# Kernel tuning notes

Measured on AMD Instinct MI355X. Metric: run time of the kernel, lower is better.

Reference implementation:

```python
import jax, jax.numpy as jnp
import numpy as np

GAMMA = 12.0
EMB_INIT = 0.05


def setup_inputs() -> dict:
    key = jax.random.key(0)
    k1, k2, k3 = jax.random.split(key, 3)
    num_chunks, chunk_size, neg_sample_size, hidden_dim = 4, 512, 256, 512
    heads = jax.random.normal(k1, (num_chunks * chunk_size, hidden_dim), dtype=jnp.float32)
    relations = jax.random.normal(k2, (num_chunks * chunk_size, hidden_dim // 2), dtype=jnp.float32)
    tails = jax.random.normal(k3, (num_chunks * neg_sample_size, hidden_dim), dtype=jnp.float32)
    return {
        "heads": heads,
        "relations": relations,
        "tails": tails,
        "num_chunks": num_chunks,
        "chunk_size": chunk_size,
        "neg_sample_size": neg_sample_size,
    }


def reference(heads, relations, tails, num_chunks, chunk_size, neg_sample_size):
    # RotatE tail-negative scoring (create_neg with neg_head=False)
    hidden_dim = heads.shape[1]
    h = hidden_dim // 2
    re_head, im_head = heads[:, :h], heads[:, h:]
    # rotate head by relation phase
    phase_rel = relations / (EMB_INIT / np.pi)
    rel_real, rel_imag = jnp.cos(phase_rel), jnp.sin(phase_rel)
    real = re_head * rel_real - im_head * rel_imag  # [nc*cs, h]
    imag = re_head * rel_imag + im_head * rel_real
    # broadcast subtract against negative tails
    tmp_r = real.reshape(num_chunks, chunk_size, 1, h)
    tmp_i = imag.reshape(num_chunks, chunk_size, 1, h)
    tails4 = tails.reshape(num_chunks, 1, neg_sample_size, hidden_dim)
    t_r, t_i = tails4[..., :h], tails4[..., h:]
    dr = tmp_r - t_r  # [nc, cs, ns, h]
    di = tmp_i - t_i
    score = jnp.sqrt(dr * dr + di * di).sum(-1)  # [nc, cs, ns]
    return GAMMA - score
```

## Files before the change

kernel.cpp:

```cpp
#include <hip/hip_runtime.h>

#define NC 4
#define CS 512
#define NS 256
#define HD 512
#define H  256
#define GAMMA_F 12.0f
#define PHASE_SCALE 62.83185307179586477f

#define KT 16

__global__ __launch_bounds__(256, 2) void score_partial(
    const float* __restrict__ heads,
    const float* __restrict__ relations,
    const float* __restrict__ tails,
    float* __restrict__ part)
{
    __shared__ float2 sh[64][KT + 1];
    __shared__ float2 st[64][KT + 1];

    int bid = blockIdx.x;
    int c    = bid >> 7;
    int rem  = bid & 127;
    int ks   = rem >> 5;
    int rem2 = rem & 31;
    int hT   = rem2 >> 2;
    int tT   = rem2 & 3;

    int hBase = c * CS + hT * 64;
    int tBase = c * NS + tT * 64;
    int kSlice = ks * 64;

    int tid = threadIdx.x;
    int tx = tid & 15;
    int ty = tid >> 4;

    int srow = tid >> 2;
    int sk   = (tid & 3) * 4;

    float acc[4][4];
    #pragma unroll
    for (int m = 0; m < 4; ++m)
        #pragma unroll
        for (int n = 0; n < 4; ++n) acc[m][n] = 0.f;

    for (int r = 0; r < 64 / KT; ++r) {
        int kBase = kSlice + r * KT;

        const float* hp = heads + (size_t)(hBase + srow) * HD + kBase + sk;
        float4 hre = *reinterpret_cast<const float4*>(hp);
        float4 him = *reinterpret_cast<const float4*>(hp + H);
        float4 rel = *reinterpret_cast<const float4*>(
            relations + (size_t)(hBase + srow) * H + kBase + sk);
        const float* tp = tails + (size_t)(tBase + srow) * HD + kBase + sk;
        float4 tre = *reinterpret_cast<const float4*>(tp);
        float4 tim = *reinterpret_cast<const float4*>(tp + H);

        __syncthreads();

        {
            float s, cc;
            __sincosf(rel.x * PHASE_SCALE, &s, &cc);
            sh[srow][sk + 0] = make_float2(hre.x * cc - him.x * s,
                                           hre.x * s + him.x * cc);
            __sincosf(rel.y * PHASE_SCALE, &s, &cc);
            sh[srow][sk + 1] = make_float2(hre.y * cc - him.y * s,
                                           hre.y * s + him.y * cc);
            __sincosf(rel.z * PHASE_SCALE, &s, &cc);
            sh[srow][sk + 2] = make_float2(hre.z * cc - him.z * s,
                                           hre.z * s + him.z * cc);
            __sincosf(rel.w * PHASE_SCALE, &s, &cc);
            sh[srow][sk + 3] = make_float2(hre.w * cc - him.w * s,
                                           hre.w * s + him.w * cc);
        }
        st[srow][sk + 0] = make_float2(tre.x, tim.x);
        st[srow][sk + 1] = make_float2(tre.y, tim.y);
        st[srow][sk + 2] = make_float2(tre.z, tim.z);
        st[srow][sk + 3] = make_float2(tre.w, tim.w);

        __syncthreads();

        #pragma unroll
        for (int kk = 0; kk < KT; ++kk) {
            float2 hv[4], tv[4];
            hv[0] = sh[ty     ][kk];
            hv[1] = sh[ty + 16][kk];
            hv[2] = sh[ty + 32][kk];
            hv[3] = sh[ty + 48][kk];
            tv[0] = st[tx     ][kk];
            tv[1] = st[tx + 16][kk];
            tv[2] = st[tx + 32][kk];
            tv[3] = st[tx + 48][kk];
            #pragma unroll
            for (int m = 0; m < 4; ++m) {
                #pragma unroll
                for (int n = 0; n < 4; ++n) {
                    float dr = hv[m].x - tv[n].x;
                    float di = hv[m].y - tv[n].y;
                    acc[m][n] += __builtin_amdgcn_sqrtf(dr * dr + di * di);
                }
            }
        }
    }

    float* plane = part + (size_t)ks * (NC * CS * NS);
    size_t cbase = (size_t)c * CS * NS;
    #pragma unroll
    for (int m = 0; m < 4; ++m) {
        int i0 = hT * 64 + ty + 16 * m;
        #pragma unroll
        for (int n = 0; n < 4; ++n) {
            int j0 = tT * 64 + tx + 16 * n;
            plane[cbase + (size_t)i0 * NS + j0] = acc[m][n];
        }
    }
}

__global__ __launch_bounds__(256) void reduce_kernel(
    const float* __restrict__ part, float* __restrict__ out)
{
    const int PLANE = NC * CS * NS;
    int idx = (blockIdx.x * 256 + threadIdx.x) * 4;
    float4 p0 = *reinterpret_cast<const float4*>(part + idx);
    float4 p1 = *reinterpret_cast<const float4*>(part + PLANE + idx);
    float4 p2 = *reinterpret_cast<const float4*>(part + 2 * PLANE + idx);
    float4 p3 = *reinterpret_cast<const float4*>(part + 3 * PLANE + idx);
    float4 r;
    r.x = GAMMA_F - (p0.x + p1.x + p2.x + p3.x);
    r.y = GAMMA_F - (p0.y + p1.y + p2.y + p3.y);
    r.z = GAMMA_F - (p0.z + p1.z + p2.z + p3.z);
    r.w = GAMMA_F - (p0.w + p1.w + p2.w + p3.w);
    *reinterpret_cast<float4*>(out + idx) = r;
}

extern "C" void kernel_launch(void* const* d_in, const int* in_sizes, int n_in,
                              void* d_out, int out_size, void* d_ws, size_t ws_size,
                              hipStream_t stream) {
    (void)in_sizes; (void)n_in; (void)ws_size; (void)out_size;
    const float* heads = (const float*)d_in[0];
    const float* rels  = (const float*)d_in[1];
    const float* tails = (const float*)d_in[2];
    float* part = (float*)d_ws;

    score_partial<<<512, 256, 0, stream>>>(heads, rels, tails, part);
    reduce_kernel<<<512, 256, 0, stream>>>(part, (float*)d_out);
}
```

Baseline: 99.69 us.

## Drop split-K partial planes; use 32x32 tiles with full-K loop and prefetch

```diff
diff --git a/kernel.cpp b/kernel.cpp
--- a/kernel.cpp
+++ b/kernel.cpp
@@ -8,55 +8,48 @@
 #define GAMMA_F 12.0f
 #define PHASE_SCALE 62.83185307179586477f
 
-#define KT 16
+#define KT 32
+#define NR (H / KT)
 
-__global__ __launch_bounds__(256, 2) void score_partial(
+__global__ __launch_bounds__(256, 2) void rotate_score(
     const float* __restrict__ heads,
     const float* __restrict__ relations,
     const float* __restrict__ tails,
-    float* __restrict__ part)
+    float* __restrict__ out)
 {
-    __shared__ float2 sh[64][KT + 1];
-    __shared__ float2 st[64][KT + 1];
+    __shared__ float2 sh[32][KT + 1];
+    __shared__ float2 st[32][KT + 1];
 
-    int bid = blockIdx.x;
-    int c    = bid >> 7;
-    int rem  = bid & 127;
-    int ks   = rem >> 5;
-    int rem2 = rem & 31;
-    int hT   = rem2 >> 2;
-    int tT   = rem2 & 3;
+    const int bid = blockIdx.x;
+    const int c   = bid >> 7;
+    const int rem = bid & 127;
+    const int hT  = rem >> 3;
+    const int tT  = rem & 7;
 
-    int hBase = c * CS + hT * 64;
-    int tBase = c * NS + tT * 64;
-    int kSlice = ks * 64;
+    const int hBase = c * CS + hT * 32;
+    const int tBase = c * NS + tT * 32;
 
-    int tid = threadIdx.x;
-    int tx = tid & 15;
-    int ty = tid >> 4;
+    const int tid = threadIdx.x;
+    const int tx  = tid & 15;
+    const int ty  = tid >> 4;
 
-    int srow = tid >> 2;
-    int sk   = (tid & 3) * 4;
+    const int srow = tid >> 3;
+    const int sk   = (tid & 7) * 4;
 
-    float acc[4][4];
-    #pragma unroll
-    for (int m = 0; m < 4; ++m)
-        #pragma unroll
-        for (int n = 0; n < 4; ++n) acc[m][n] = 0.f;
+    const float* hp0 = heads     + (size_t)(hBase + srow) * HD + sk;
+    const float* rp0 = relations + (size_t)(hBase + srow) * H  + sk;
+    const float* tp0 = tails     + (size_t)(tBase + srow) * HD + sk;
 
-    for (int r = 0; r < 64 / KT; ++r) {
-        int kBase = kSlice + r * KT;
+    float4 hre = *reinterpret_cast<const float4*>(hp0);
+    float4 him = *reinterpret_cast<const float4*>(hp0 + H);
+    float4 rel = *reinterpret_cast<const float4*>(rp0);
+    float4 tre = *reinterpret_cast<const float4*>(tp0);
+    float4 tim = *reinterpret_cast<const float4*>(tp0 + H);
 
-        const float* hp = heads + (size_t)(hBase + srow) * HD + kBase + sk;
-        float4 hre = *reinterpret_cast<const float4*>(hp);
-        float4 him = *reinterpret_cast<const float4*>(hp + H);
-        float4 rel = *reinterpret_cast<const float4*>(
-            relations + (size_t)(hBase + srow) * H + kBase + sk);
-        const float* tp = tails + (size_t)(tBase + srow) * HD + kBase + sk;
-        float4 tre = *reinterpret_cast<const float4*>(tp);
-        float4 tim = *reinterpret_cast<const float4*>(tp + H);
+    float acc00 = 0.f, acc01 = 0.f, acc10 = 0.f, acc11 = 0.f;
 
-        __syncthreads();
+    for (int r = 0; r < NR; ++r) {
+        if (r) __syncthreads();
 
         {
             float s, cc;
@@ -80,68 +73,49 @@
 
         __syncthreads();
 
+        if (r + 1 < NR) {
+            const int kOff = (r + 1) * KT;
+            hre = *reinterpret_cast<const float4*>(hp0 + kOff);
+            him = *reinterpret_cast<const float4*>(hp0 + H + kOff);
+            rel = *reinterpret_cast<const float4*>(rp0 + kOff);
+            tre = *reinterpret_cast<const float4*>(tp0 + kOff);
+            tim = *reinterpret_cast<const float4*>(tp0 + H + kOff);
+        }
+
         #pragma unroll
         for (int kk = 0; kk < KT; ++kk) {
-            float2 hv[4], tv[4];
-            hv[0] = sh[ty     ][kk];
-            hv[1] = sh[ty + 16][kk];
-            hv[2] = sh[ty + 32][kk];
-            hv[3] = sh[ty + 48][kk];
-            tv[0] = st[tx     ][kk];
-            tv[1] = st[tx + 16][kk];
-            tv[2] = st[tx + 32][kk];
-            tv[3] = st[tx + 48][kk];
-            #pragma unroll
-            for (int m = 0; m < 4; ++m) {
-                #pragma unroll
-                for (int n = 0; n < 4; ++n) {
-                    float dr = hv[m].x - tv[n].x;
-                    float di = hv[m].y - tv[n].y;
-                    acc[m][n] += __builtin_amdgcn_sqrtf(dr * dr + di * di);
-                }
-            }
+            float2 h0 = sh[ty     ][kk];
+            float2 h1 = sh[ty + 16][kk];
+            float2 t0 = st[tx     ][kk];
+            float2 t1 = st[tx + 16][kk];
+            float dr, di;
+            dr = h0.x - t0.x; di = h0.y - t0.y;
+            acc00 += __builtin_amdgcn_sqrtf(fmaf(dr, dr, di * di));
+            dr = h0.x - t1.x; di = h0.y - t1.y;
+            acc01 += __builtin_amdgcn_sqrtf(fmaf(dr, dr, di * di));
+            dr = h1.x - t0.x; di = h1.y - t0.y;
+            acc10 += __builtin_amdgcn_sqrtf(fmaf(dr, dr, di * di));
+            dr = h1.x - t1.x; di = h1.y - t1.y;
+            acc11 += __builtin_amdgcn_sqrtf(fmaf(dr, dr, di * di));
         }
     }
 
-    float* plane = part + (size_t)ks * (NC * CS * NS);
-    size_t cbase = (size_t)c * CS * NS;
-    #pragma unroll
-    for (int m = 0; m < 4; ++m) {
-        int i0 = hT * 64 + ty + 16 * m;
-        #pragma unroll
-        for (int n = 0; n < 4; ++n) {
-            int j0 = tT * 64 + tx + 16 * n;
-            plane[cbase + (size_t)i0 * NS + j0] = acc[m][n];
-        }
-    }
-}
-
-__global__ __launch_bounds__(256) void reduce_kernel(
-    const float* __restrict__ part, float* __restrict__ out)
-{
-    const int PLANE = NC * CS * NS;
-    int idx = (blockIdx.x * 256 + threadIdx.x) * 4;
-    float4 p0 = *reinterpret_cast<const float4*>(part + idx);
-    float4 p1 = *reinterpret_cast<const float4*>(part + PLANE + idx);
-    float4 p2 = *reinterpret_cast<const float4*>(part + 2 * PLANE + idx);
-    float4 p3 = *reinterpret_cast<const float4*>(part + 3 * PLANE + idx);
-    float4 r;
-    r.x = GAMMA_F - (p0.x + p1.x + p2.x + p3.x);
-    r.y = GAMMA_F - (p0.y + p1.y + p2.y + p3.y);
-    r.z = GAMMA_F - (p0.z + p1.z + p2.z + p3.z);
-    r.w = GAMMA_F - (p0.w + p1.w + p2.w + p3.w);
-    *reinterpret_cast<float4*>(out + idx) = r;
+    const size_t cbase = (size_t)c * CS * NS;
+    const int i0 = hT * 32 + ty;
+    const int j0 = tT * 32 + tx;
+    out[cbase + (size_t)i0        * NS + j0     ] = GAMMA_F - acc00;
+    out[cbase + (size_t)i0        * NS + j0 + 16] = GAMMA_F - acc01;
+    out[cbase + (size_t)(i0 + 16) * NS + j0     ] = GAMMA_F - acc10;
+    out[cbase + (size_t)(i0 + 16) * NS + j0 + 16] = GAMMA_F - acc11;
 }
 
 extern "C" void kernel_launch(void* const* d_in, const int* in_sizes, int n_in,
                               void* d_out, int out_size, void* d_ws, size_t ws_size,
                               hipStream_t stream) {
-    (void)in_sizes; (void)n_in; (void)ws_size; (void)out_size;
+    (void)in_sizes; (void)n_in; (void)ws_size; (void)out_size; (void)d_ws;
     const float* heads = (const float*)d_in[0];
     const float* rels  = (const float*)d_in[1];
     const float* tails = (const float*)d_in[2];
-    float* part = (float*)d_ws;
 
-    score_partial<<<512, 256, 0, stream>>>(heads, rels, tails, part);
-    reduce_kernel<<<512, 256, 0, stream>>>(part, (float*)d_out);
+    rotate_score<<<512, 256, 0, stream>>>(heads, rels, tails, (float*)d_out);
 }
```

After: 97.74 us. No clear change (-2.0%).
